# Kernel optimization log

Hardware: AMD Instinct MI355X
Metric: run time of the kernel (lower is better)

## Reference

```python
import jax, jax.numpy as jnp
import numpy as np

HEADS = 8
GS = 16
C = 512
E = 512
SCALE = (E / HEADS) ** -0.5
PNAMES = ['sa_qkv_w','sa_qkv_b','sa_pa_w','sa_pa_b','sa_ln1_g','sa_ln1_b','sa_f1_w','sa_f1_b','sa_f2_w','sa_f2_b','sa_ln2_g','sa_ln2_b','sa_c1_w','sa_c1_b','sa_c2_w','sa_c2_b','sa_bn_g','sa_bn_b','ca_q_w','ca_q_b','ca_k_w','ca_k_b','ca_v_w','ca_v_b','ca_pa_w','ca_pa_b','p_q_w','p_q_b','p_k_w','p_k_b','p_v_w','p_v_b','p_pa_w','p_pa_b','p_ln_g','p_ln_b','p_lin_w','p_lin_b']


def _ln(x, g, b, eps=1e-5):
    m = x.mean(-1, keepdims=True)
    v = jnp.var(x, axis=-1, keepdims=True)
    return (x - m) / jnp.sqrt(v + eps) * g + b


def _conv1x1(x, w, b):
    return jnp.einsum('bchw,oc->bohw', x, w) + b[None, :, None, None]


def _up_ac(x, out=GS):
    # bilinear upsample, align_corners=True (nn.UpsamplingBilinear2d)
    H = x.shape[2]
    pos = jnp.arange(out) * (H - 1) / (out - 1)
    lo = jnp.floor(pos).astype(jnp.int32)
    hi = jnp.minimum(lo + 1, H - 1)
    w = (pos - lo).astype(x.dtype)
    xr = x[:, :, lo, :] * (1 - w)[None, None, :, None] + x[:, :, hi, :] * w[None, None, :, None]
    return xr[:, :, :, lo] * (1 - w) + xr[:, :, :, hi] * w


def _asri(x, p):
    # Sequence_ASRI: GAP tokens -> attention over the batch axis -> pixel-shuffle back
    B = x.shape[0]; ch = E // HEADS
    gap = x.mean((2, 3))                                             # [B,C]
    qkv = (gap @ p['sa_qkv_w'].T + p['sa_qkv_b']).reshape(B, 4, ch, HEADS).transpose(1, 3, 0, 2)  # [4,H,B,ch]
    q, k, v, skip = qkv[0], qkv[1], qkv[2], qkv[3]
    attn = jax.nn.softmax(jnp.einsum('hbc,hdc->hbd', q, k) * SCALE, -1)  # [H,B,B]
    o = jnp.einsum('hbd,hdc->hbc', attn, v)
    merge = lambda t: t.transpose(1, 2, 0).reshape(B, E)             # 'head b c -> b (c head)'
    a = merge(o) @ p['sa_pa_w'].T + p['sa_pa_b'] + merge(skip)
    h = jax.nn.relu(_ln(a, p['sa_ln1_g'], p['sa_ln1_b']) @ p['sa_f1_w'].T + p['sa_f1_b'])
    a = h @ p['sa_f2_w'].T + p['sa_f2_b'] + a
    s = _ln(a, p['sa_ln2_g'], p['sa_ln2_b']) @ p['sa_c1_w'].T + p['sa_c1_b']  # [B,C*16]
    s = _up_ac(s.reshape(B, C, 4, 4))                                 # pixel shuffle p1=p2=4 then bilinear to 16x16
    s = _conv1x1(s, p['sa_c2_w'], p['sa_c2_b'])
    # BatchNorm2d in eval mode (running_mean=0, running_var=1, eps=1e-5)
    s = s / np.float32(np.sqrt(1.0 + 1e-5)) * p['sa_bn_g'][None, :, None, None] + p['sa_bn_b'][None, :, None, None]
    return x + jax.nn.relu(s)


def _sscm(x1, x2, p):
    # Sequence_SSCM: GAP-token q/k over batch axis, full spatial v
    B = x1.shape[0]; ch = E // HEADS
    q = (x1.mean((2, 3)) @ p['ca_q_w'].T + p['ca_q_b']).reshape(B, ch, HEADS).transpose(2, 0, 1)  # [H,B,ch]
    k = (x2.mean((2, 3)) @ p['ca_k_w'].T + p['ca_k_b']).reshape(B, ch, HEADS).transpose(2, 0, 1)
    v = _conv1x1(x2, p['ca_v_w'], p['ca_v_b']).reshape(B, ch, HEADS, GS, GS).transpose(2, 0, 1, 3, 4).reshape(HEADS, B, ch * GS * GS)
    attn = jax.nn.softmax(jnp.einsum('hbc,hdc->hbd', q, k) * SCALE, -1)  # [H,B,B]
    o = jnp.einsum('hbd,hdm->hbm', attn, v)
    o = o.reshape(HEADS, B, ch, GS, GS).transpose(1, 2, 0, 3, 4).reshape(B, E, GS, GS)
    return jax.nn.relu(_conv1x1(o, p['ca_pa_w'], p['ca_pa_b']))


def _pixel(x1, x2, p):
    # Pixel_SSCM: pixel-wise cross-batch attention (no scale -- matches source)
    B = x1.shape[0]; ch = E // HEADS; N = GS * GS
    split = lambda t: t.reshape(B, ch, HEADS, N).transpose(2, 0, 3, 1)   # 'b (c head) h w -> head b (h w) c'
    q = split(_conv1x1(x1, p['p_q_w'], p['p_q_b']))                      # [H,B,N,ch]
    k = split(_conv1x1(x2, p['p_k_w'], p['p_k_b']))
    v = split(_conv1x1(x2, p['p_v_w'], p['p_v_b'])).reshape(HEADS, B * N, ch)
    attn = jax.nn.softmax(jnp.einsum('hbnc,hqmc->hbqnm', q, k), -1)      # [H,B,B,N,N]
    attn = attn.transpose(1, 0, 3, 2, 4).reshape(B, HEADS, N, B * N)     # 'head b q h w -> b head h (q w)'
    o = jnp.einsum('bhnm,hmc->bhnc', attn, v)
    o = o.transpose(0, 3, 1, 2).reshape(B, E, GS, GS)                    # 'b head (h w) c -> b (c head) h w'
    o = _conv1x1(o, p['p_pa_w'], p['p_pa_b']) + x1
    t = o.reshape(B, C, N).transpose(0, 2, 1)                            # [B,N,C]
    t = jax.nn.relu(_ln(t, p['p_ln_g'], p['p_ln_b']) @ p['p_lin_w'].T + p['p_lin_b'])
    return t.transpose(0, 2, 1).reshape(B, C, GS, GS)


def _hrlm(p, xs, xq):
    sa_s = _asri(xs, p)
    sa_q = _asri(xq, p)
    ca_s = _sscm(sa_s, sa_q, p)
    ca_q = _sscm(sa_q, sa_s, p)
    return _pixel(sa_s, ca_q, p), _pixel(sa_q, ca_s, p)


def setup_inputs():
    key = jax.random.key(0)
    ks = iter(jax.random.split(key, 64))
    w = lambda *s: (jax.random.normal(next(ks), s) * 0.02).astype(jnp.float32)
    z = lambda n: jnp.zeros((n,), jnp.float32)
    o = lambda n: jnp.ones((n,), jnp.float32)
    return dict(
        fea_support=jax.random.normal(next(ks), (8, C, GS, GS), jnp.float32),
        fea_query=jax.random.normal(next(ks), (8, C, GS, GS), jnp.float32),
        sa_qkv_w=w(4 * E, C), sa_qkv_b=z(4 * E),
        sa_pa_w=w(E, E), sa_pa_b=z(E),
        sa_ln1_g=o(E), sa_ln1_b=z(E),
        sa_f1_w=w(E, E), sa_f1_b=z(E), sa_f2_w=w(E, E), sa_f2_b=z(E),
        sa_ln2_g=o(E), sa_ln2_b=z(E),
        sa_c1_w=w(C * 16, E), sa_c1_b=z(C * 16),
        sa_c2_w=w(C, E), sa_c2_b=z(C),
        sa_bn_g=o(C), sa_bn_b=z(C),
        ca_q_w=w(E, C), ca_q_b=z(E), ca_k_w=w(E, C), ca_k_b=z(E),
        ca_v_w=w(E, C), ca_v_b=z(E), ca_pa_w=w(C, E), ca_pa_b=z(C),
        p_q_w=w(E, C), p_q_b=z(E), p_k_w=w(E, C), p_k_b=z(E),
        p_v_w=w(E, C), p_v_b=z(E), p_pa_w=w(C, E), p_pa_b=z(C),
        p_ln_g=o(C), p_ln_b=z(C), p_lin_w=w(C, C), p_lin_b=z(C),
    )


def reference(fea_support, fea_query, sa_qkv_w, sa_qkv_b, sa_pa_w, sa_pa_b, sa_ln1_g, sa_ln1_b, sa_f1_w, sa_f1_b, sa_f2_w, sa_f2_b, sa_ln2_g, sa_ln2_b, sa_c1_w, sa_c1_b, sa_c2_w, sa_c2_b, sa_bn_g, sa_bn_b, ca_q_w, ca_q_b, ca_k_w, ca_k_b, ca_v_w, ca_v_b, ca_pa_w, ca_pa_b, p_q_w, p_q_b, p_k_w, p_k_b, p_v_w, p_v_b, p_pa_w, p_pa_b, p_ln_g, p_ln_b, p_lin_w, p_lin_b):
    p = dict(zip(PNAMES, (sa_qkv_w, sa_qkv_b, sa_pa_w, sa_pa_b, sa_ln1_g, sa_ln1_b, sa_f1_w, sa_f1_b, sa_f2_w, sa_f2_b, sa_ln2_g, sa_ln2_b, sa_c1_w, sa_c1_b, sa_c2_w, sa_c2_b, sa_bn_g, sa_bn_b, ca_q_w, ca_q_b, ca_k_w, ca_k_b, ca_v_w, ca_v_b, ca_pa_w, ca_pa_b, p_q_w, p_q_b, p_k_w, p_k_b, p_v_w, p_v_b, p_pa_w, p_pa_b, p_ln_g, p_ln_b, p_lin_w, p_lin_b)))
    return _hrlm(p, fea_support, fea_query)
```

## Files before the change

### kernel.cpp

```cpp
#include <hip/hip_runtime.h>
#include <cmath>

#define IMG 131072
#define BIGF 1048576

#define CF_RELU  1
#define CF_RES   2
#define CF_BN    4
#define CF_SPLIT 8
#define CF_TRANS 16

typedef __attribute__((ext_vector_type(8))) short short8;
typedef __attribute__((ext_vector_type(4))) short short4v;
typedef __attribute__((ext_vector_type(4))) float f32x4;

__device__ __forceinline__ float wave_sum(float v){
    #pragma unroll
    for (int off = 32; off; off >>= 1) v += __shfl_xor(v, off);
    return v;
}

__device__ __forceinline__ unsigned short bf16_rn(float x){
    union { float f; unsigned u; } v; v.f = x;
    unsigned r = v.u + 0x7FFF + ((v.u >> 16) & 1);
    return (unsigned short)(r >> 16);
}
__device__ __forceinline__ float bf16_to_f(unsigned short h){
    union { float f; unsigned u; } v; v.u = ((unsigned)h) << 16;
    return v.f;
}
__device__ __forceinline__ unsigned pack_split(float x){
    unsigned short hi = bf16_rn(x);
    unsigned short lo = bf16_rn(x - bf16_to_f(hi));
    return (unsigned)hi | ((unsigned)lo << 16);
}
__device__ __forceinline__ unsigned pk_hi(unsigned a, unsigned b){
    return __builtin_amdgcn_perm(b, a, 0x05040100u);
}
__device__ __forceinline__ unsigned pk_lo(unsigned a, unsigned b){
    return __builtin_amdgcn_perm(b, a, 0x07060302u);
}

struct GapJobs  { const float* x[2]; float* o[2]; };
struct G8Job    { const float* in; const float* W; const float* bias; const float* add; float* out; };
struct G8Jobs   { G8Job j[4]; };
struct AAJobs   { const float* qkv[2]; float* om[2]; };
struct LnJobs   { const float* in[2]; float* out[2]; };
struct UpJobs   { const float* in[2]; float* out[2]; };
struct SAJobs   { const float* q8[2]; const float* k8[2]; float* aw[2]; };
struct SPJobs   { const float* aw[2]; const float* v[2]; float* out[2]; };
struct ZJobs    { float* p[2]; };
struct ConvJob  { const float* X; const float* X2; const float* W; const float* B; const float* R;
                  const float* bng; const float* bnb; float* O; int flags; };
struct ConvJobs { ConvJob j[6]; };
struct PixJob   { const unsigned* Q; const unsigned* K; const unsigned* V; float* Oa; float* Ob; };
struct PixJobs  { PixJob j[2]; };

__global__ __launch_bounds__(64) void k_gap(GapJobs jo){
    const int br = blockIdx.y;
    const int bc = blockIdx.x;
    const int lane = threadIdx.x;
    const float* p = jo.x[br] + (size_t)bc * 256;
    float s = p[lane] + p[lane + 64] + p[lane + 128] + p[lane + 192];
    s = wave_sum(s);
    if (lane == 0) jo.o[br][bc] = s * (1.0f / 256.0f);
}

__global__ __launch_bounds__(64) void k_gemm8(G8Jobs jo, int add_off, int add_stride, int O, int relu){
    const G8Job j = jo.j[blockIdx.y];
    const int o = blockIdx.x;
    const int lane = threadIdx.x;
    const float* wr = j.W + (size_t)o * 512;
    float acc[8] = {0,0,0,0,0,0,0,0};
    #pragma unroll
    for (int i = 0; i < 8; i++){
        float w = wr[lane + 64*i];
        #pragma unroll
        for (int b = 0; b < 8; b++) acc[b] += w * j.in[b*512 + lane + 64*i];
    }
    #pragma unroll
    for (int b = 0; b < 8; b++) acc[b] = wave_sum(acc[b]);
    if (lane < 8){
        float v = acc[0];
        #pragma unroll
        for (int b = 1; b < 8; b++) if (lane == b) v = acc[b];
        v += j.bias[o];
        if (j.add) v += j.add[lane*add_stride + add_off + o];
        if (relu) v = fmaxf(v, 0.f);
        j.out[(size_t)lane * O + o] = v;
    }
}

__global__ __launch_bounds__(64) void k_asri_attn(AAJobs jo){
    const int br = blockIdx.y;
    const float* qkv = jo.qkv[br];
    const int h = blockIdx.x >> 3, b = blockIdx.x & 7, c = threadIdx.x;
    const int ci = c*8 + h;
    float qc = qkv[b*2048 + ci];
    float s[8];
    #pragma unroll
    for (int d = 0; d < 8; d++){
        float p = qc * qkv[d*2048 + 512 + ci];
        p = wave_sum(p);
        s[d] = p * 0.125f;
    }
    float m = s[0];
    #pragma unroll
    for (int d = 1; d < 8; d++) m = fmaxf(m, s[d]);
    float sum = 0.f;
    #pragma unroll
    for (int d = 0; d < 8; d++){ s[d] = __expf(s[d]-m); sum += s[d]; }
    float r = 1.f / sum;
    float oc = 0.f;
    #pragma unroll
    for (int d = 0; d < 8; d++) oc += s[d]*r * qkv[d*2048 + 1024 + ci];
    jo.om[br][b*512 + ci] = oc;
}

__global__ __launch_bounds__(64) void k_ln8(LnJobs jo,
    const float* __restrict__ g, const float* __restrict__ be)
{
    const int br = blockIdx.y;
    const int b = blockIdx.x, lane = threadIdx.x;
    const float* in = jo.in[br];
    float v[8]; float s = 0.f;
    #pragma unroll
    for (int i = 0; i < 8; i++){ v[i] = in[b*512 + lane + 64*i]; s += v[i]; }
    s = wave_sum(s);
    float mean = s * (1.f/512.f);
    float q = 0.f;
    #pragma unroll
    for (int i = 0; i < 8; i++){ float d = v[i]-mean; q += d*d; }
    q = wave_sum(q);
    float rstd = rsqrtf(q*(1.f/512.f) + 1e-5f);
    #pragma unroll
    for (int i = 0; i < 8; i++){
        int c = lane + 64*i;
        jo.out[br][b*512 + c] = (v[i]-mean)*rstd*g[c] + be[c];
    }
}

__global__ __launch_bounds__(256) void k_up(UpJobs jo){
    const int br = blockIdx.y;
    const int idx = blockIdx.x*256 + threadIdx.x;
    const int x = idx & 15, y = (idx >> 4) & 15, bc = idx >> 8;
    float px = (float)(x*3) / 15.0f, py = (float)(y*3) / 15.0f;
    int lx = (int)px, ly = (int)py;
    float wx = px - lx, wy = py - ly;
    int hx = min(lx+1, 3), hy = min(ly+1, 3);
    const float* p = jo.in[br] + (size_t)bc * 16;
    float v00 = p[ly*4+lx], v01 = p[ly*4+hx], v10 = p[hy*4+lx], v11 = p[hy*4+hx];
    float a0 = v00*(1.f-wy) + v10*wy;
    float a1 = v01*(1.f-wy) + v11*wy;
    jo.out[br][idx] = a0*(1.f-wx) + a1*wx;
}

__global__ __launch_bounds__(256) void k_zero(ZJobs jo){
    jo.p[blockIdx.y][(size_t)blockIdx.x*256 + threadIdx.x] = 0.f;
}

#define LDK 40
__device__ __forceinline__ void convm_body(
    const float* __restrict__ Xb, const float* __restrict__ X2b,
    const float* __restrict__ W,
    const float* __restrict__ bias, const float* __restrict__ resb,
    const float* __restrict__ bng, const float* __restrict__ bnb, float bninv,
    float* __restrict__ outb, int flags, int o0, int n0, unsigned short* lds)
{
    const int tid512 = threadIdx.x;
    const int g   = tid512 >> 8;
    const int tid = tid512 & 255;
    unsigned short* sAh = lds + g*10240;
    unsigned short* sAl = sAh + 2560;
    unsigned short* sBh = sAl + 2560;
    unsigned short* sBl = sBh + 2560;
    const int wv = tid >> 6, lane = tid & 63;
    const int quad = lane >> 4, l16 = lane & 15;
    const int wo = (wv >> 1) * 32, wn = (wv & 1) * 32;
    const int so  = tid >> 2, sk8 = (tid & 3) * 8;
    const int sp  = tid & 15, sn  = (tid >> 4) * 4;

    const bool trans = (flags & CF_TRANS) != 0;
    int so_g = o0 + so;
    if (trans) so_g = ((so_g & 63) << 3) | (so_g >> 6);

    const float* wrow = W + (size_t)so_g*512 + g*256 + sk8;
    const size_t xoff = (size_t)(g*256 + 2*sp)*256 + n0 + sn;
    const float* xrow  = Xb + xoff;
    const float* x2row = X2b ? X2b + xoff : nullptr;

    auto ldx4 = [&](size_t off){
        float4 v = *(const float4*)(xrow + off);
        if (x2row){
            float4 w2 = *(const float4*)(x2row + off);
            v.x += w2.x; v.y += w2.y; v.z += w2.z; v.w += w2.w;
        }
        return v;
    };

    f32x4 acc[2][2] = {};
    float4 a0 = *(const float4*)(wrow);
    float4 a1 = *(const float4*)(wrow + 4);
    float4 x0 = ldx4(0);
    float4 x1 = ldx4(256);

    for (int k0 = 0; k0 < 256; k0 += 32){
        __syncthreads();
        {
            float wa[8] = {a0.x,a0.y,a0.z,a0.w,a1.x,a1.y,a1.z,a1.w};
            #pragma unroll
            for (int j = 0; j < 4; j++){
                unsigned short h0 = bf16_rn(wa[2*j]);
                unsigned short h1 = bf16_rn(wa[2*j+1]);
                unsigned short g0 = bf16_rn(wa[2*j]   - bf16_to_f(h0));
                unsigned short g1 = bf16_rn(wa[2*j+1] - bf16_to_f(h1));
                *(unsigned*)&sAh[so*LDK + sk8 + 2*j] = (unsigned)h0 | ((unsigned)h1 << 16);
                *(unsigned*)&sAl[so*LDK + sk8 + 2*j] = (unsigned)g0 | ((unsigned)g1 << 16);
            }
            float xe[4] = {x0.x,x0.y,x0.z,x0.w};
            float xo[4] = {x1.x,x1.y,x1.z,x1.w};
            #pragma unroll
            for (int j = 0; j < 4; j++){
                unsigned short h0 = bf16_rn(xe[j]);
                unsigned short h1 = bf16_rn(xo[j]);
                unsigned short g0 = bf16_rn(xe[j] - bf16_to_f(h0));
                unsigned short g1 = bf16_rn(xo[j] - bf16_to_f(h1));
                *(unsigned*)&sBh[(sn+j)*LDK + 2*sp] = (unsigned)h0 | ((unsigned)h1 << 16);
                *(unsigned*)&sBl[(sn+j)*LDK + 2*sp] = (unsigned)g0 | ((unsigned)g1 << 16);
            }
        }
        __syncthreads();
        if (k0 + 32 < 256){
            a0 = *(const float4*)(wrow + k0 + 32);
            a1 = *(const float4*)(wrow + k0 + 36);
            x0 = ldx4((size_t)(k0+32)*256);
            x1 = ldx4((size_t)(k0+32)*256 + 256);
        }
        short8 ah[2], al[2], bh[2], bl[2];
        #pragma unroll
        for (int t = 0; t < 2; t++){
            int ai = (wo + 16*t + l16)*LDK + quad*8;
            ah[t] = *(const short8*)&sAh[ai];
            al[t] = *(const short8*)&sAl[ai];
            int bi = (wn + 16*t + l16)*LDK + quad*8;
            bh[t] = *(const short8*)&sBh[bi];
            bl[t] = *(const short8*)&sBl[bi];
        }
        if (trans){
            #pragma unroll
            for (int mt = 0; mt < 2; mt++){
                #pragma unroll
                for (int nt = 0; nt < 2; nt++){
                    acc[mt][nt] = __builtin_amdgcn_mfma_f32_16x16x32_bf16(bh[nt], ah[mt], acc[mt][nt], 0, 0, 0);
                    acc[mt][nt] = __builtin_amdgcn_mfma_f32_16x16x32_bf16(bl[nt], ah[mt], acc[mt][nt], 0, 0, 0);
                    acc[mt][nt] = __builtin_amdgcn_mfma_f32_16x16x32_bf16(bh[nt], al[mt], acc[mt][nt], 0, 0, 0);
                }
            }
        } else {
            #pragma unroll
            for (int mt = 0; mt < 2; mt++){
                #pragma unroll
                for (int nt = 0; nt < 2; nt++){
                    acc[mt][nt] = __builtin_amdgcn_mfma_f32_16x16x32_bf16(ah[mt], bh[nt], acc[mt][nt], 0, 0, 0);
                    acc[mt][nt] = __builtin_amdgcn_mfma_f32_16x16x32_bf16(ah[mt], bl[nt], acc[mt][nt], 0, 0, 0);
                    acc[mt][nt] = __builtin_amdgcn_mfma_f32_16x16x32_bf16(al[mt], bh[nt], acc[mt][nt], 0, 0, 0);
                }
            }
        }
    }
    __syncthreads();
    float* red = (float*)lds;
    if (g == 1){
        float* r = red + tid*20;
        #pragma unroll
        for (int mt = 0; mt < 2; mt++)
            #pragma unroll
            for (int nt = 0; nt < 2; nt++)
                *(f32x4*)(r + (mt*2+nt)*4) = acc[mt][nt];
    }
    __syncthreads();
    if (g == 0){
        float* r = red + tid*20;
        #pragma unroll
        for (int mt = 0; mt < 2; mt++)
            #pragma unroll
            for (int nt = 0; nt < 2; nt++){
                f32x4 o4 = *(const f32x4*)(r + (mt*2+nt)*4);
                acc[mt][nt] += o4;
            }
        if (trans){
            unsigned* op = (unsigned*)outb;
            #pragma unroll
            for (int mt = 0; mt < 2; mt++){
                #pragma unroll
                for (int nt = 0; nt < 2; nt++){
                    const int p  = o0 + wo + 16*mt + l16;
                    const int nb = n0 + wn + 16*nt + quad*4;
                    const int osrc = ((p & 63) << 3) | (p >> 6);
                    const float bs = bias[osrc];
                    #pragma unroll
                    for (int rr = 0; rr < 4; rr++){
                        float v = acc[mt][nt][rr] + bs;
                        op[(size_t)(nb+rr)*512 + p] = pack_split(v);
                    }
                }
            }
        } else {
            #pragma unroll
            for (int mt = 0; mt < 2; mt++){
                #pragma unroll
                for (int nt = 0; nt < 2; nt++){
                    const int n  = n0 + wn + 16*nt + l16;
                    const int ob = o0 + wo + 16*mt + quad*4;
                    #pragma unroll
                    for (int rr = 0; rr < 4; rr++){
                        const int o = ob + rr;
                        float v = acc[mt][nt][rr] + bias[o];
                        if (flags & CF_BN)   v = v*(bninv*bng[o]) + bnb[o];
                        if (flags & CF_RELU) v = fmaxf(v, 0.f);
                        if (flags & CF_RES)  v += resb[(size_t)o*256 + n];
                        if (flags & CF_SPLIT){
                            ((unsigned*)outb)[(size_t)o*256 + n] = pack_split(v);
                        } else {
                            outb[(size_t)o*256 + n] = v;
                        }
                    }
                }
            }
        }
    }
}

__global__ __launch_bounds__(512) void k_convm(ConvJobs jo, float bninv)
{
    __shared__ unsigned short lds[20480];
    const int z = blockIdx.z;
    const ConvJob j = jo.j[z >> 3];
    const int b = z & 7;
    convm_body(j.X + (size_t)b*IMG,
               j.X2 ? j.X2 + (size_t)b*IMG : nullptr,
               j.W, j.B,
               j.R ? j.R + (size_t)b*IMG : nullptr,
               j.bng, j.bnb, bninv,
               j.O + (size_t)b*IMG, j.flags,
               blockIdx.y*64, blockIdx.x*64, lds);
}

__global__ __launch_bounds__(64) void k_sscm_attn(SAJobs jo)
{
    const int br = blockIdx.y;
    const int h = blockIdx.x >> 3, b = blockIdx.x & 7, c = threadIdx.x;
    const int ci = c*8 + h;
    float qc = jo.q8[br][b*512 + ci];
    float s[8];
    #pragma unroll
    for (int d = 0; d < 8; d++){
        float p = qc * jo.k8[br][d*512 + ci];
        p = wave_sum(p);
        s[d] = p * 0.125f;
    }
    float m = s[0];
    #pragma unroll
    for (int d = 1; d < 8; d++) m = fmaxf(m, s[d]);
    float sum = 0.f;
    #pragma unroll
    for (int d = 0; d < 8; d++){ s[d] = __expf(s[d]-m); sum += s[d]; }
    float r = 1.f/sum;
    if (c < 8){
        float v = s[0];
        #pragma unroll
        for (int d = 1; d < 8; d++) if (c == d) v = s[d];
        jo.aw[br][blockIdx.x*8 + c] = v*r;
    }
}

__global__ __launch_bounds__(256) void k_sscm_apply(SPJobs jo)
{
    const int br = blockIdx.y;
    const int idx = blockIdx.x*256 + threadIdx.x;
    const int pix = idx & 255, e = (idx >> 8) & 511, b = idx >> 17;
    const int h = e & 7;
    const float* aw = jo.aw[br] + (h*8 + b)*8;
    const float* v = jo.v[br];
    float acc = 0.f;
    #pragma unroll
    for (int d = 0; d < 8; d++) acc += aw[d] * v[(size_t)d*IMG + (size_t)e*256 + pix];
    jo.out[br][idx] = acc;
}

__global__ __launch_bounds__(256) void k_pixel_mfma(PixJobs jo)
{
    __shared__ char smem[40960];
    unsigned short* sQh = (unsigned short*)smem;
    unsigned short* sQl = sQh + 2*64*40;
    unsigned short* sKh = sQl + 2*64*40;
    unsigned short* sKl = sKh + 2*64*40;
    unsigned short* sP  = (unsigned short*)smem;
    unsigned short* sVh = sKh;
    unsigned short* sVl = sKl;

    const int br = blockIdx.y >> 3, b = blockIdx.y & 7;
    const PixJob J = jo.j[br];
    const int nt = blockIdx.x & 3, dg = blockIdx.x >> 2;
    const int h = blockIdx.z;
    const int tid = threadIdx.x;
    const int wv = tid >> 6, lane = tid & 63;
    const int quad = lane >> 4, l16 = lane & 15;
    const int n0 = nt * 64;

    {
        const unsigned* Qt = J.Q + (size_t)b*IMG + (size_t)n0*512 + h*64;
        const int q = tid >> 2, i0 = (tid & 3) * 16;
        const unsigned* src = Qt + (size_t)q*512 + i0;
        uint4 w0 = *(const uint4*)(src);
        uint4 w1 = *(const uint4*)(src + 4);
        uint4 w2 = *(const uint4*)(src + 8);
        uint4 w3 = *(const uint4*)(src + 12);
        unsigned hb[8], lb[8];
        hb[0]=pk_hi(w0.x,w0.y); hb[1]=pk_hi(w0.z,w0.w); hb[2]=pk_hi(w1.x,w1.y); hb[3]=pk_hi(w1.z,w1.w);
        hb[4]=pk_hi(w2.x,w2.y); hb[5]=pk_hi(w2.z,w2.w); hb[6]=pk_hi(w3.x,w3.y); hb[7]=pk_hi(w3.z,w3.w);
        lb[0]=pk_lo(w0.x,w0.y); lb[1]=pk_lo(w0.z,w0.w); lb[2]=pk_lo(w1.x,w1.y); lb[3]=pk_lo(w1.z,w1.w);
        lb[4]=pk_lo(w2.x,w2.y); lb[5]=pk_lo(w2.z,w2.w); lb[6]=pk_lo(w3.x,w3.y); lb[7]=pk_lo(w3.z,w3.w);
        int dst = (i0>>5)*2560 + q*40 + (i0&31);
        *(uint4*)&sQh[dst]     = *(uint4*)&hb[0];
        *(uint4*)&sQh[dst + 8] = *(uint4*)&hb[4];
        *(uint4*)&sQl[dst]     = *(uint4*)&lb[0];
        *(uint4*)&sQl[dst + 8] = *(uint4*)&lb[4];
    }
    __syncthreads();

    short8 bqh[2], bql[2];
    #pragma unroll
    for (int ks = 0; ks < 2; ks++){
        int idx = ks*2560 + (wv*16 + l16)*40 + quad*8;
        bqh[ks] = *(const short8*)&sQh[idx];
        bql[ks] = *(const short8*)&sQl[idx];
    }

    const int mloc = tid & 63, cb0 = tid >> 6;
    const int mp = tid & 31,  c0v = tid >> 5;
    uint4 pf[4];

    auto loadK = [&](int d, int mq){
        const unsigned* Kt = J.K + (size_t)d*IMG + (size_t)(mq*64 + mloc)*512 + h*64;
        pf[0] = *(const uint4*)(Kt + cb0*8);
        pf[1] = *(const uint4*)(Kt + cb0*8 + 4);
        pf[2] = *(const uint4*)(Kt + (cb0+4)*8);
        pf[3] = *(const uint4*)(Kt + (cb0+4)*8 + 4);
    };
    auto writeK = [&](){
        #pragma unroll
        for (int p = 0; p < 2; p++){
            uint4 wa = pf[2*p], wb = pf[2*p+1];
            union { short8 s; unsigned u[4]; } hu, lu;
            hu.u[0]=pk_hi(wa.x,wa.y); hu.u[1]=pk_hi(wa.z,wa.w);
            hu.u[2]=pk_hi(wb.x,wb.y); hu.u[3]=pk_hi(wb.z,wb.w);
            lu.u[0]=pk_lo(wa.x,wa.y); lu.u[1]=pk_lo(wa.z,wa.w);
            lu.u[2]=pk_lo(wb.x,wb.y); lu.u[3]=pk_lo(wb.z,wb.w);
            int cb = cb0 + 4*p;
            int idx = (cb>>2)*2560 + mloc*40 + (cb&3)*8;
            *(short8*)&sKh[idx] = hu.s;
            *(short8*)&sKl[idx] = lu.s;
        }
    };
    auto loadV = [&](int d, int vs){
        const unsigned* Vp = J.V + (size_t)d*IMG + (size_t)h*256 + (vs>>1)*128 + (vs&1)*64 + 2*mp;
        #pragma unroll
        for (int p2 = 0; p2 < 4; p2++){
            uint2 wA = *(const uint2*)(Vp + (size_t)(c0v + 16*p2)*2048);
            uint2 wB = *(const uint2*)(Vp + (size_t)(c0v + 16*p2 + 8)*2048);
            pf[p2].x = wA.x; pf[p2].y = wA.y; pf[p2].z = wB.x; pf[p2].w = wB.y;
        }
    };
    auto writeV = [&](){
        const int ib = ((2*mp)>>5)*2560 + ((2*mp)&31);
        #pragma unroll
        for (int p2 = 0; p2 < 4; p2++){
            int ca = c0v + 16*p2, cb2 = ca + 8;
            *(unsigned*)&sVh[ib + ca*40]  = pk_hi(pf[p2].x, pf[p2].y);
            *(unsigned*)&sVl[ib + ca*40]  = pk_lo(pf[p2].x, pf[p2].y);
            *(unsigned*)&sVh[ib + cb2*40] = pk_hi(pf[p2].z, pf[p2].w);
            *(unsigned*)&sVl[ib + cb2*40] = pk_lo(pf[p2].z, pf[p2].w);
        }
    };

    f32x4 oac[4] = {};
    loadK(dg*4, 0);

    for (int dd = 0; dd < 4; dd++){
        const int d = dg*4 + dd;

        f32x4 S[16] = {};
        #pragma unroll
        for (int mq = 0; mq < 4; mq++){
            if (mq | dd) __syncthreads();
            writeK();
            if (mq < 3) loadK(d, mq+1);
            else        loadV(d, 0);
            __syncthreads();
            __builtin_amdgcn_s_setprio(1);
            #pragma unroll
            for (int mtl = 0; mtl < 4; mtl++){
                int t = mq*4 + mtl;
                #pragma unroll
                for (int ks = 0; ks < 2; ks++){
                    int idx = ks*2560 + (mtl*16 + l16)*40 + quad*8;
                    short8 ah = *(const short8*)&sKh[idx];
                    short8 al = *(const short8*)&sKl[idx];
                    S[t] = __builtin_amdgcn_mfma_f32_16x16x32_bf16(ah, bqh[ks], S[t], 0, 0, 0);
                    S[t] = __builtin_amdgcn_mfma_f32_16x16x32_bf16(ah, bql[ks], S[t], 0, 0, 0);
                    S[t] = __builtin_amdgcn_mfma_f32_16x16x32_bf16(al, bqh[ks], S[t], 0, 0, 0);
                }
            }
            __builtin_amdgcn_s_setprio(0);
        }

        {
            float mx = -3.4e38f;
            #pragma unroll
            for (int t = 0; t < 16; t++)
                #pragma unroll
                for (int r = 0; r < 4; r++) mx = fmaxf(mx, S[t][r]);
            mx = fmaxf(mx, __shfl_xor(mx, 16));
            mx = fmaxf(mx, __shfl_xor(mx, 32));
            float sum = 0.f;
            #pragma unroll
            for (int t = 0; t < 16; t++)
                #pragma unroll
                for (int r = 0; r < 4; r++){ S[t][r] = __expf(S[t][r]-mx); sum += S[t][r]; }
            sum += __shfl_xor(sum, 16);
            sum += __shfl_xor(sum, 32);
            float rr = 1.f/sum;
            #pragma unroll
            for (int t = 0; t < 16; t++)
                #pragma unroll
                for (int r = 0; r < 4; r++) S[t][r] *= rr;
        }

        #pragma unroll
        for (int vs = 0; vs < 4; vs++){
            __syncthreads();
            if ((vs & 1) == 0){
                const int hm = vs >> 1;
                #pragma unroll
                for (int mtl = 0; mtl < 8; mtl++){
                    int t = hm*8 + mtl;
                    short4v p4;
                    #pragma unroll
                    for (int r = 0; r < 4; r++) p4[r] = (short)bf16_rn(S[t][r]);
                    int idx = (mtl>>1)*2560 + (wv*16 + l16)*40 + 16*(mtl&1) + quad*4;
                    *(short4v*)&sP[idx] = p4;
                }
            }
            writeV();
            if (vs < 3)      loadV(d, vs+1);
            else if (dd < 3) loadK(d+1, 0);
            __syncthreads();
            __builtin_amdgcn_s_setprio(1);
            #pragma unroll
            for (int l = 0; l < 2; l++){
                int gks = (vs & 1)*2 + l;
                int pidx = gks*2560 + (wv*16 + l16)*40 + quad*8;
                short8 bp = *(const short8*)&sP[pidx];
                #pragma unroll
                for (int ct = 0; ct < 4; ct++){
                    int vidx = l*2560 + (ct*16 + l16)*40 + quad*8;
                    short8 vh = *(const short8*)&sVh[vidx];
                    short8 vl = *(const short8*)&sVl[vidx];
                    oac[ct] = __builtin_amdgcn_mfma_f32_16x16x32_bf16(vh, bp, oac[ct], 0, 0, 0);
                    oac[ct] = __builtin_amdgcn_mfma_f32_16x16x32_bf16(vl, bp, oac[ct], 0, 0, 0);
                }
            }
            __builtin_amdgcn_s_setprio(0);
        }
    }

    {
        float* base = (J.Ob ? (dg ? J.Ob : J.Oa) : J.Oa);
        float* Obp = base + (size_t)b * IMG;
        const int q = n0 + wv*16 + l16;
        if (J.Ob){
            #pragma unroll
            for (int ct = 0; ct < 4; ct++){
                #pragma unroll
                for (int r = 0; r < 4; r++){
                    int c = ct*16 + quad*4 + r;
                    Obp[(size_t)(c*8+h)*256 + q] = oac[ct][r];
                }
            }
        } else {
            #pragma unroll
            for (int ct = 0; ct < 4; ct++){
                #pragma unroll
                for (int r = 0; r < 4; r++){
                    int c = ct*16 + quad*4 + r;
                    unsafeAtomicAdd(&Obp[(size_t)(c*8+h)*256 + q], oac[ct][r]);
                }
            }
        }
    }
}

__global__ __launch_bounds__(64) void k_ln_pix(LnJobs jo,
    const float* __restrict__ g, const float* __restrict__ be)
{
    const int br = blockIdx.y;
    const int bn = blockIdx.x;
    const int b = bn >> 8, n = bn & 255;
    const int lane = threadIdx.x;
    const float* p = jo.in[br] + (size_t)b*IMG + n;
    float v[8]; float s = 0.f;
    #pragma unroll
    for (int i = 0; i < 8; i++){ v[i] = p[(size_t)(lane + 64*i)*256]; s += v[i]; }
    s = wave_sum(s);
    float mean = s * (1.f/512.f);
    float q = 0.f;
    #pragma unroll
    for (int i = 0; i < 8; i++){ float d = v[i]-mean; q += d*d; }
    q = wave_sum(q);
    float rstd = rsqrtf(q*(1.f/512.f) + 1e-5f);
    #pragma unroll
    for (int i = 0; i < 8; i++){
        int c = lane + 64*i;
        jo.out[br][(size_t)b*IMG + (size_t)c*256 + n] = (v[i]-mean)*rstd*g[c] + be[c];
    }
}

extern "C" void kernel_launch(void* const* d_in, const int* in_sizes, int n_in,
                              void* d_out, int out_size, void* d_ws, size_t ws_size,
                              hipStream_t stream)
{
    const float* xs    = (const float*)d_in[0];
    const float* xq    = (const float*)d_in[1];
    const float* qkvw  = (const float*)d_in[2];  const float* qkvb = (const float*)d_in[3];
    const float* paw   = (const float*)d_in[4];  const float* pab  = (const float*)d_in[5];
    const float* ln1g  = (const float*)d_in[6];  const float* ln1b = (const float*)d_in[7];
    const float* f1w   = (const float*)d_in[8];  const float* f1b  = (const float*)d_in[9];
    const float* f2w   = (const float*)d_in[10]; const float* f2b  = (const float*)d_in[11];
    const float* ln2g  = (const float*)d_in[12]; const float* ln2b = (const float*)d_in[13];
    const float* c1w   = (const float*)d_in[14]; const float* c1b  = (const float*)d_in[15];
    const float* c2w   = (const float*)d_in[16]; const float* c2b  = (const float*)d_in[17];
    const float* bng   = (const float*)d_in[18]; const float* bnb  = (const float*)d_in[19];
    const float* caqw  = (const float*)d_in[20]; const float* caqb = (const float*)d_in[21];
    const float* cakw  = (const float*)d_in[22]; const float* cakb = (const float*)d_in[23];
    const float* cavw  = (const float*)d_in[24]; const float* cavb = (const float*)d_in[25];
    const float* capw  = (const float*)d_in[26]; const float* capb = (const float*)d_in[27];
    const float* pqw   = (const float*)d_in[28]; const float* pqb  = (const float*)d_in[29];
    const float* pkw   = (const float*)d_in[30]; const float* pkb  = (const float*)d_in[31];
    const float* pvw   = (const float*)d_in[32]; const float* pvb  = (const float*)d_in[33];
    const float* ppw   = (const float*)d_in[34]; const float* ppb  = (const float*)d_in[35];
    const float* plng  = (const float*)d_in[36]; const float* plnb = (const float*)d_in[37];
    const float* plinw = (const float*)d_in[38]; const float* plinb= (const float*)d_in[39];

    const size_t SMF = 262144;
    float* ws = (float*)d_ws;
    float* smb = ws;
    float* B[14];
    for (int i = 0; i < 14; i++) B[i] = ws + SMF + (size_t)i*BIGF;
    float* sa_s = B[0]; float* sa_q = B[1];
    float* ca_s = B[2]; float* ca_q = B[3];
    const bool paired_pixel = ws_size >= (SMF + 12*(size_t)BIGF)*sizeof(float) + 1024;
    const bool has_dsplit   = ws_size >= (SMF + 14*(size_t)BIGF)*sizeof(float) + 1024;

    auto SM = [&](int br){ return smb + (size_t)br*131072; };
    auto GAP=[&](int br){ return SM(br); };            auto QKV=[&](int br){ return SM(br)+4096; };
    auto OM =[&](int br){ return SM(br)+20480; };      auto AA =[&](int br){ return SM(br)+24576; };
    auto HB =[&](int br){ return SM(br)+28672; };      auto A2 =[&](int br){ return SM(br)+32768; };
    auto LNB=[&](int br){ return SM(br)+36864; };      auto S8 =[&](int br){ return SM(br)+40960; };
    auto ATW=[&](int br){ return SM(br)+106496; };     auto Q8 =[&](int br){ return SM(br)+107008; };
    auto K8 =[&](int br){ return SM(br)+111104; };

    const float bninv = 1.0f / sqrtf(1.0f + 1e-5f);
    float* out0 = (float*)d_out;
    float* out1 = out0 + (size_t)BIGF;

    {
        GapJobs gj = {{xs, xq}, {GAP(0), GAP(1)}};
        k_gap<<<dim3(4096,2), 64, 0, stream>>>(gj);
        G8Jobs qj = {{{GAP(0), qkvw, qkvb, nullptr, QKV(0)}, {GAP(1), qkvw, qkvb, nullptr, QKV(1)}}};
        k_gemm8<<<dim3(2048,2), 64, 0, stream>>>(qj, 0, 0, 2048, 0);
        AAJobs aj = {{QKV(0), QKV(1)}, {OM(0), OM(1)}};
        k_asri_attn<<<dim3(64,2), 64, 0, stream>>>(aj);
        G8Jobs pj = {{{OM(0), paw, pab, QKV(0), AA(0)}, {OM(1), paw, pab, QKV(1), AA(1)}}};
        k_gemm8<<<dim3(512,2), 64, 0, stream>>>(pj, 1536, 2048, 512, 0);
        LnJobs l1 = {{AA(0), AA(1)}, {LNB(0), LNB(1)}};
        k_ln8<<<dim3(8,2), 64, 0, stream>>>(l1, ln1g, ln1b);
        G8Jobs fj = {{{LNB(0), f1w, f1b, nullptr, HB(0)}, {LNB(1), f1w, f1b, nullptr, HB(1)}}};
        k_gemm8<<<dim3(512,2), 64, 0, stream>>>(fj, 0, 0, 512, 1);
        G8Jobs f2j = {{{HB(0), f2w, f2b, AA(0), A2(0)}, {HB(1), f2w, f2b, AA(1), A2(1)}}};
        k_gemm8<<<dim3(512,2), 64, 0, stream>>>(f2j, 0, 512, 512, 0);
        LnJobs l2 = {{A2(0), A2(1)}, {LNB(0), LNB(1)}};
        k_ln8<<<dim3(8,2), 64, 0, stream>>>(l2, ln2g, ln2b);
        G8Jobs cj = {{{LNB(0), c1w, c1b, nullptr, S8(0)}, {LNB(1), c1w, c1b, nullptr, S8(1)}}};
        k_gemm8<<<dim3(8192,2), 64, 0, stream>>>(cj, 0, 0, 8192, 0);
        UpJobs uj = {{S8(0), S8(1)}, {B[4], B[5]}};
        k_up<<<dim3(4096,2), 256, 0, stream>>>(uj);
        ConvJobs c2j = {};
        c2j.j[0] = {B[4], nullptr, c2w, c2b, xs, bng, bnb, sa_s, CF_BN|CF_RELU|CF_RES};
        c2j.j[1] = {B[5], nullptr, c2w, c2b, xq, bng, bnb, sa_q, CF_BN|CF_RELU|CF_RES};
        k_convm<<<dim3(4,8,16), 512, 0, stream>>>(c2j, bninv);
    }

    {
        GapJobs gj = {{sa_s, sa_q}, {GAP(0), GAP(1)}};
        k_gap<<<dim3(4096,2), 64, 0, stream>>>(gj);
        G8Jobs qj = {{{GAP(0), caqw, caqb, nullptr, Q8(0)},
                      {GAP(1), cakw, cakb, nullptr, K8(0)},
                      {GAP(1), caqw, caqb, nullptr, Q8(1)},
                      {GAP(0), cakw, cakb, nullptr, K8(1)}}};
        k_gemm8<<<dim3(512,4), 64, 0, stream>>>(qj, 0, 0, 512, 0);
        SAJobs sj = {{Q8(0), Q8(1)}, {K8(0), K8(1)}, {ATW(0), ATW(1)}};
        k_sscm_attn<<<dim3(64,2), 64, 0, stream>>>(sj);
        ConvJobs vj = {};
        vj.j[0] = {sa_q, nullptr, cavw, cavb, nullptr, nullptr, nullptr, B[4], 0};
        vj.j[1] = {sa_s, nullptr, cavw, cavb, nullptr, nullptr, nullptr, B[5], 0};
        k_convm<<<dim3(4,8,16), 512, 0, stream>>>(vj, 1.f);
        SPJobs pj = {{ATW(0), ATW(1)}, {B[4], B[5]}, {B[6], B[7]}};
        k_sscm_apply<<<dim3(4096,2), 256, 0, stream>>>(pj);
        ConvJobs aj = {};
        aj.j[0] = {B[6], nullptr, capw, capb, nullptr, nullptr, nullptr, ca_s, CF_RELU};
        aj.j[1] = {B[7], nullptr, capw, capb, nullptr, nullptr, nullptr, ca_q, CF_RELU};
        k_convm<<<dim3(4,8,16), 512, 0, stream>>>(aj, 1.f);
    }

    if (paired_pixel){
        ConvJobs qkvj = {};
        qkvj.j[0] = {sa_s, nullptr, pqw, pqb, nullptr, nullptr, nullptr, B[4],  CF_SPLIT|CF_TRANS};
        qkvj.j[1] = {ca_q, nullptr, pkw, pkb, nullptr, nullptr, nullptr, B[5],  CF_SPLIT|CF_TRANS};
        qkvj.j[2] = {ca_q, nullptr, pvw, pvb, nullptr, nullptr, nullptr, B[6],  CF_SPLIT};
        qkvj.j[3] = {sa_q, nullptr, pqw, pqb, nullptr, nullptr, nullptr, B[8],  CF_SPLIT|CF_TRANS};
        qkvj.j[4] = {ca_s, nullptr, pkw, pkb, nullptr, nullptr, nullptr, B[9],  CF_SPLIT|CF_TRANS};
        qkvj.j[5] = {ca_s, nullptr, pvw, pvb, nullptr, nullptr, nullptr, B[10], CF_SPLIT};
        k_convm<<<dim3(4,8,48), 512, 0, stream>>>(qkvj, 1.f);
        if (!has_dsplit){
            ZJobs zj = {{B[7], B[11]}};
            k_zero<<<dim3(4096,2), 256, 0, stream>>>(zj);
        }
        float* o2a = has_dsplit ? B[12] : nullptr;
        float* o2b = has_dsplit ? B[13] : nullptr;
        PixJobs pxj = {{{(const unsigned*)B[4], (const unsigned*)B[5], (const unsigned*)B[6],  B[7],  o2a},
                        {(const unsigned*)B[8], (const unsigned*)B[9], (const unsigned*)B[10], B[11], o2b}}};
        k_pixel_mfma<<<dim3(8,16,8), 256, 0, stream>>>(pxj);
        ConvJobs ppj = {};
        ppj.j[0] = {B[7],  o2a, ppw, ppb, sa_s, nullptr, nullptr, out0, CF_RES};
        ppj.j[1] = {B[11], o2b, ppw, ppb, sa_q, nullptr, nullptr, out1, CF_RES};
        k_convm<<<dim3(4,8,16), 512, 0, stream>>>(ppj, 1.f);
        LnJobs lj = {{out0, out1}, {B[4], B[8]}};
        k_ln_pix<<<dim3(2048,2), 64, 0, stream>>>(lj, plng, plnb);
        ConvJobs lnj = {};
        lnj.j[0] = {B[4], nullptr, plinw, plinb, nullptr, nullptr, nullptr, out0, CF_RELU};
        lnj.j[1] = {B[8], nullptr, plinw, plinb, nullptr, nullptr, nullptr, out1, CF_RELU};
        k_convm<<<dim3(4,8,16), 512, 0, stream>>>(lnj, 1.f);
    } else {
        auto pixel1 = [&](const float* x1, const float* x2, float* out){
            ConvJobs qkvj = {};
            qkvj.j[0] = {x1, nullptr, pqw, pqb, nullptr, nullptr, nullptr, B[4], CF_SPLIT|CF_TRANS};
            qkvj.j[1] = {x2, nullptr, pkw, pkb, nullptr, nullptr, nullptr, B[5], CF_SPLIT|CF_TRANS};
            qkvj.j[2] = {x2, nullptr, pvw, pvb, nullptr, nullptr, nullptr, B[6], CF_SPLIT};
            k_convm<<<dim3(4,8,24), 512, 0, stream>>>(qkvj, 1.f);
            ZJobs zj = {{B[7], B[7]}};
            k_zero<<<dim3(4096,1), 256, 0, stream>>>(zj);
            PixJobs pxj = {{{(const unsigned*)B[4], (const unsigned*)B[5], (const unsigned*)B[6], B[7], nullptr},
                            {(const unsigned*)B[4], (const unsigned*)B[5], (const unsigned*)B[6], B[7], nullptr}}};
            k_pixel_mfma<<<dim3(8,8,8), 256, 0, stream>>>(pxj);
            ConvJobs ppj = {};
            ppj.j[0] = {B[7], nullptr, ppw, ppb, x1, nullptr, nullptr, out, CF_RES};
            k_convm<<<dim3(4,8,8), 512, 0, stream>>>(ppj, 1.f);
            LnJobs lj = {{out, out}, {B[4], B[4]}};
            k_ln_pix<<<dim3(2048,1), 64, 0, stream>>>(lj, plng, plnb);
            ConvJobs lnj = {};
            lnj.j[0] = {B[4], nullptr, plinw, plinb, nullptr, nullptr, nullptr, out, CF_RELU};
            k_convm<<<dim3(4,8,8), 512, 0, stream>>>(lnj, 1.f);
        };
        pixel1(sa_s, ca_q, out0);
        pixel1(sa_q, ca_s, out1);
    }

    (void)in_sizes; (void)n_in; (void)out_size;
}
```

Baseline: 473.5 us.

## Add smaller-tile split-bf16 MFMA 1x1 conv kernel for non-split conv launches

```diff
diff --git a/kernel.cpp b/kernel.cpp
--- a/kernel.cpp
+++ b/kernel.cpp
@@ -344,6 +344,122 @@
                j.bng, j.bnb, bninv,
                j.O + (size_t)b*IMG, j.flags,
                blockIdx.y*64, blockIdx.x*64, lds);
+}
+
+__global__ __launch_bounds__(256) void k_convm2(ConvJobs jo, float bninv)
+{
+    __shared__ unsigned short lds[7680];
+    const int z = blockIdx.z;
+    const ConvJob j = jo.j[z >> 3];
+    const int b = z & 7;
+    const float* Xb   = j.X + (size_t)b*IMG;
+    const float* X2b  = j.X2 ? j.X2 + (size_t)b*IMG : nullptr;
+    const float* resb = j.R  ? j.R  + (size_t)b*IMG : nullptr;
+    float* outb = j.O + (size_t)b*IMG;
+    const int o0 = blockIdx.y*32, n0 = blockIdx.x*64;
+    const int flags = j.flags;
+
+    unsigned short* sAh = lds;
+    unsigned short* sAl = lds + 1280;
+    unsigned short* sBh = lds + 2560;
+    unsigned short* sBl = lds + 5120;
+    const int tid = threadIdx.x;
+    const int wv = tid >> 6, lane = tid & 63;
+    const int quad = lane >> 4, l16 = lane & 15;
+    const int wo = (wv >> 1) * 16, wn = (wv & 1) * 32;
+    const int so = tid >> 3, sk = (tid & 7) * 4;
+    const int sp = tid & 15, sn = (tid >> 4) * 4;
+
+    const float* wrow = j.W + (size_t)(o0 + so)*512 + sk;
+    const size_t xoff = (size_t)(2*sp)*256 + n0 + sn;
+    const float* xrow  = Xb + xoff;
+    const float* x2row = X2b ? X2b + xoff : nullptr;
+
+    auto ldx4 = [&](size_t off){
+        float4 v = *(const float4*)(xrow + off);
+        if (x2row){
+            float4 w2 = *(const float4*)(x2row + off);
+            v.x += w2.x; v.y += w2.y; v.z += w2.z; v.w += w2.w;
+        }
+        return v;
+    };
+
+    f32x4 acc[2] = {};
+    float4 a0 = *(const float4*)(wrow);
+    float4 x0 = ldx4(0);
+    float4 x1 = ldx4(256);
+
+    for (int k0 = 0; k0 < 512; k0 += 32){
+        __syncthreads();
+        {
+            unsigned short h0 = bf16_rn(a0.x);
+            unsigned short h1 = bf16_rn(a0.y);
+            unsigned short g0 = bf16_rn(a0.x - bf16_to_f(h0));
+            unsigned short g1 = bf16_rn(a0.y - bf16_to_f(h1));
+            *(unsigned*)&sAh[so*40 + sk]     = (unsigned)h0 | ((unsigned)h1 << 16);
+            *(unsigned*)&sAl[so*40 + sk]     = (unsigned)g0 | ((unsigned)g1 << 16);
+            h0 = bf16_rn(a0.z);
+            h1 = bf16_rn(a0.w);
+            g0 = bf16_rn(a0.z - bf16_to_f(h0));
+            g1 = bf16_rn(a0.w - bf16_to_f(h1));
+            *(unsigned*)&sAh[so*40 + sk + 2] = (unsigned)h0 | ((unsigned)h1 << 16);
+            *(unsigned*)&sAl[so*40 + sk + 2] = (unsigned)g0 | ((unsigned)g1 << 16);
+
+            float xe[4] = {x0.x,x0.y,x0.z,x0.w};
+            float xo[4] = {x1.x,x1.y,x1.z,x1.w};
+            #pragma unroll
+            for (int jj = 0; jj < 4; jj++){
+                unsigned short e0 = bf16_rn(xe[jj]);
+                unsigned short e1 = bf16_rn(xo[jj]);
+                unsigned short f0 = bf16_rn(xe[jj] - bf16_to_f(e0));
+                unsigned short f1 = bf16_rn(xo[jj] - bf16_to_f(e1));
+                *(unsigned*)&sBh[(sn+jj)*40 + 2*sp] = (unsigned)e0 | ((unsigned)e1 << 16);
+                *(unsigned*)&sBl[(sn+jj)*40 + 2*sp] = (unsigned)f0 | ((unsigned)f1 << 16);
+            }
+        }
+        __syncthreads();
+        if (k0 + 32 < 512){
+            a0 = *(const float4*)(wrow + k0 + 32);
+            x0 = ldx4((size_t)(k0+32)*256);
+            x1 = ldx4((size_t)(k0+32)*256 + 256);
+        }
+        short8 ah, al, bh0, bl0, bh1, bl1;
+        {
+            int ai = (wo + l16)*40 + quad*8;
+            ah = *(const short8*)&sAh[ai];
+            al = *(const short8*)&sAl[ai];
+        }
+        {
+            int bi = (wn + l16)*40 + quad*8;
+            bh0 = *(const short8*)&sBh[bi];
+            bl0 = *(const short8*)&sBl[bi];
+        }
+        {
+            int bi = (wn + 16 + l16)*40 + quad*8;
+            bh1 = *(const short8*)&sBh[bi];
+            bl1 = *(const short8*)&sBl[bi];
+        }
+        acc[0] = __builtin_amdgcn_mfma_f32_16x16x32_bf16(ah, bh0, acc[0], 0, 0, 0);
+        acc[0] = __builtin_amdgcn_mfma_f32_16x16x32_bf16(ah, bl0, acc[0], 0, 0, 0);
+        acc[0] = __builtin_amdgcn_mfma_f32_16x16x32_bf16(al, bh0, acc[0], 0, 0, 0);
+        acc[1] = __builtin_amdgcn_mfma_f32_16x16x32_bf16(ah, bh1, acc[1], 0, 0, 0);
+        acc[1] = __builtin_amdgcn_mfma_f32_16x16x32_bf16(ah, bl1, acc[1], 0, 0, 0);
+        acc[1] = __builtin_amdgcn_mfma_f32_16x16x32_bf16(al, bh1, acc[1], 0, 0, 0);
+    }
+    #pragma unroll
+    for (int nt = 0; nt < 2; nt++){
+        const int n  = n0 + wn + 16*nt + l16;
+        const int ob = o0 + wo + quad*4;
+        #pragma unroll
+        for (int rr = 0; rr < 4; rr++){
+            const int o = ob + rr;
+            float v = acc[nt][rr] + j.B[o];
+            if (flags & CF_BN)   v = v*(bninv*j.bng[o]) + j.bnb[o];
+            if (flags & CF_RELU) v = fmaxf(v, 0.f);
+            if (flags & CF_RES)  v += resb[(size_t)o*256 + n];
+            outb[(size_t)o*256 + n] = v;
+        }
+    }
 }
 
 __global__ __launch_bounds__(64) void k_sscm_attn(SAJobs jo)
@@ -698,7 +814,7 @@
         ConvJobs c2j = {};
         c2j.j[0] = {B[4], nullptr, c2w, c2b, xs, bng, bnb, sa_s, CF_BN|CF_RELU|CF_RES};
         c2j.j[1] = {B[5], nullptr, c2w, c2b, xq, bng, bnb, sa_q, CF_BN|CF_RELU|CF_RES};
-        k_convm<<<dim3(4,8,16), 512, 0, stream>>>(c2j, bninv);
+        k_convm2<<<dim3(4,16,16), 256, 0, stream>>>(c2j, bninv);
     }
 
     {
@@ -714,13 +830,13 @@
         ConvJobs vj = {};
         vj.j[0] = {sa_q, nullptr, cavw, cavb, nullptr, nullptr, nullptr, B[4], 0};
         vj.j[1] = {sa_s, nullptr, cavw, cavb, nullptr, nullptr, nullptr, B[5], 0};
-        k_convm<<<dim3(4,8,16), 512, 0, stream>>>(vj, 1.f);
+        k_convm2<<<dim3(4,16,16), 256, 0, stream>>>(vj, 1.f);
         SPJobs pj = {{ATW(0), ATW(1)}, {B[4], B[5]}, {B[6], B[7]}};
         k_sscm_apply<<<dim3(4096,2), 256, 0, stream>>>(pj);
         ConvJobs aj = {};
         aj.j[0] = {B[6], nullptr, capw, capb, nullptr, nullptr, nullptr, ca_s, CF_RELU};
         aj.j[1] = {B[7], nullptr, capw, capb, nullptr, nullptr, nullptr, ca_q, CF_RELU};
-        k_convm<<<dim3(4,8,16), 512, 0, stream>>>(aj, 1.f);
+        k_convm2<<<dim3(4,16,16), 256, 0, stream>>>(aj, 1.f);
     }
 
     if (paired_pixel){
@@ -744,13 +860,13 @@
         ConvJobs ppj = {};
         ppj.j[0] = {B[7],  o2a, ppw, ppb, sa_s, nullptr, nullptr, out0, CF_RES};
         ppj.j[1] = {B[11], o2b, ppw, ppb, sa_q, nullptr, nullptr, out1, CF_RES};
-        k_convm<<<dim3(4,8,16), 512, 0, stream>>>(ppj, 1.f);
+        k_convm2<<<dim3(4,16,16), 256, 0, stream>>>(ppj, 1.f);
         LnJobs lj = {{out0, out1}, {B[4], B[8]}};
         k_ln_pix<<<dim3(2048,2), 64, 0, stream>>>(lj, plng, plnb);
         ConvJobs lnj = {};
         lnj.j[0] = {B[4], nullptr, plinw, plinb, nullptr, nullptr, nullptr, out0, CF_RELU};
         lnj.j[1] = {B[8], nullptr, plinw, plinb, nullptr, nullptr, nullptr, out1, CF_RELU};
-        k_convm<<<dim3(4,8,16), 512, 0, stream>>>(lnj, 1.f);
+        k_convm2<<<dim3(4,16,16), 256, 0, stream>>>(lnj, 1.f);
     } else {
         auto pixel1 = [&](const float* x1, const float* x2, float* out){
             ConvJobs qkvj = {};
@@ -765,12 +881,12 @@
             k_pixel_mfma<<<dim3(8,8,8), 256, 0, stream>>>(pxj);
             ConvJobs ppj = {};
             ppj.j[0] = {B[7], nullptr, ppw, ppb, x1, nullptr, nullptr, out, CF_RES};
-            k_convm<<<dim3(4,8,8), 512, 0, stream>>>(ppj, 1.f);
+            k_convm2<<<dim3(4,16,8), 256, 0, stream>>>(ppj, 1.f);
             LnJobs lj = {{out, out}, {B[4], B[4]}};
             k_ln_pix<<<dim3(2048,1), 64, 0, stream>>>(lj, plng, plnb);
             ConvJobs lnj = {};
             lnj.j[0] = {B[4], nullptr, plinw, plinb, nullptr, nullptr, nullptr, out, CF_RELU};
-            k_convm<<<dim3(4,8,8), 512, 0, stream>>>(lnj, 1.f);
+            k_convm2<<<dim3(4,16,8), 256, 0, stream>>>(lnj, 1.f);
         };
         pixel1(sa_s, ca_q, out0);
         pixel1(sa_q, ca_s, out1);
```

Result: slower. 495.3 us (+4.6%).
